# Kernel optimization log

Hardware: AMD Instinct MI355X
Metric: run time of the kernel (lower is better)

## Reference

```python
import jax, jax.numpy as jnp
import numpy as np

B, S, H = 256, 4096, 64

def setup_inputs() -> dict:
    key = jax.random.key(0)
    ks = jax.random.split(key, 6)
    x = jax.random.normal(ks[0], (B, S), dtype=jnp.float32)
    # e = nn.Linear(1, H)
    W_e = jax.random.normal(ks[1], (H, 1), dtype=jnp.float32)
    b_e = jax.random.normal(ks[2], (H,), dtype=jnp.float32) * 0.01
    # PhaseAccumulator learnable per-unit frequency
    omega = 1.0 + 0.1 * jax.random.normal(ks[3], (H,), dtype=jnp.float32)
    # r = nn.Linear(3*H, 1)
    W_r = jax.random.normal(ks[4], (1, 3 * H), dtype=jnp.float32) * (1.0 / np.sqrt(3 * H))
    b_r = jnp.zeros((1,), dtype=jnp.float32)
    return {"x": x, "W_e": W_e, "b_e": b_e, "omega": omega, "W_r": W_r, "b_r": b_r}

def reference(x, W_e, b_e, omega, W_r, b_r):
    # per-step 1->H linear, vectorized over all timesteps: p[b,s,h]
    p = x[:, :, None] * W_e[:, 0] + b_e                 # [B,S,H]
    # xp = stack([cos p, sin p]); accumulator delta = atan2(sin p, cos p) = wrap(p)
    delta = jnp.arctan2(jnp.sin(p), jnp.cos(p))         # [B,S,H], wrapped to (-pi, pi]
    # ph_t = ph_{t-1} + omega * delta_t, ph_0 = 0  ->  cumulative sum over time
    Hseq = jnp.cumsum(omega * delta, axis=1)            # [B,S,H] all phase states
    ph = Hseq[:, -1]                                    # [B,H] final phase
    feat = jnp.concatenate([jnp.cos(ph), jnp.sin(ph), ph], axis=1)  # [B,3H]
    out = feat @ W_r.T + b_r                            # [B,1]
    return out, Hseq
```

## Files before the change

kernel.cpp:

```cpp
#include <hip/hip_runtime.h>

#define B_SZ   256
#define S_SZ   4096
#define H_SZ   64
#define NCHUNK 32
#define CHUNK  (S_SZ / NCHUNK)

#define INV2PI   0.15915494309189535f
#define TWOPI_HI 6.2831854820251465f
#define TWOPI_LO (-1.7484556000744887e-7f)

__device__ __forceinline__ const float* uniform_ptr(const float* p) {
    uint64_t u = (uint64_t)(uintptr_t)p;
    uint32_t lo = __builtin_amdgcn_readfirstlane((uint32_t)u);
    uint32_t hi = __builtin_amdgcn_readfirstlane((uint32_t)(u >> 32));
    return (const float*)(uintptr_t)(((uint64_t)hi << 32) | lo);
}

__global__ __launch_bounds__(256, 4) void k_partials(
    const float* __restrict__ x, const float* __restrict__ W_e,
    const float* __restrict__ b_e, float* __restrict__ ws)
{
    int tid   = blockIdx.x * 256 + threadIdx.x;
    int wid   = tid >> 6;
    int lane  = threadIdx.x & 63;
    int b     = wid >> 5;
    int chunk = wid & (NCHUNK - 1);

    float we = W_e[lane];
    float be = b_e[lane];

    const float* xpu = uniform_ptr(x + b * S_SZ + chunk * CHUNK);
    float accN = 0.f;
    float accX = 0.f;
    #pragma unroll 16
    for (int j = 0; j < CHUNK; ++j) {
        float xs = xpu[j];
        float p  = fmaf(xs, we, be);
        accN += rintf(p * INV2PI);
        accX += xs;
    }
    float sP = fmaf(we, accX, (float)CHUNK * be);
    float d  = fmaf(accN, -TWOPI_HI, sP);
    d        = fmaf(accN, -TWOPI_LO, d);
    ws[wid * 64 + lane] = d;
}

__global__ __launch_bounds__(256, 4) void k_scan(
    const float* __restrict__ x, const float* __restrict__ W_e,
    const float* __restrict__ b_e, const float* __restrict__ omega,
    const float* __restrict__ W_r, const float* __restrict__ b_r,
    const float* __restrict__ ws, float* __restrict__ out,
    float* __restrict__ hseq)
{
    int tid   = blockIdx.x * 256 + threadIdx.x;
    int wid   = tid >> 6;
    int lane  = threadIdx.x & 63;
    int b     = wid >> 5;
    int chunk = wid & (NCHUNK - 1);

    float we = W_e[lane];
    float be = b_e[lane];
    float om = omega[lane];

    float base = 0.f;
    for (int c = 0; c < chunk; ++c)
        base += ws[(b * NCHUNK + c) * 64 + lane];
    float obase = om * base;

    const float* xpu = uniform_ptr(x + b * S_SZ + chunk * CHUNK);
    float* hp = hseq + (size_t)(b * S_SZ + chunk * CHUNK) * H_SZ + lane;

    float acc  = 0.f;
    float Hval = obase;
    #pragma unroll 16
    for (int j = 0; j < CHUNK; ++j) {
        float xs = xpu[j];
        float p  = fmaf(xs, we, be);
        float n  = rintf(p * INV2PI);
        float d0 = fmaf(n, -TWOPI_HI, p);
        d0       = fmaf(n, -TWOPI_LO, d0);
        acc += d0;
        Hval = fmaf(om, acc, obase);
        __builtin_nontemporal_store(Hval, hp + (size_t)j * H_SZ);
    }

    if (chunk == NCHUNK - 1) {
        float ph = Hval;
        float v = cosf(ph) * W_r[lane]
                + sinf(ph) * W_r[H_SZ + lane]
                + ph       * W_r[2 * H_SZ + lane];
        #pragma unroll
        for (int off = 32; off > 0; off >>= 1)
            v += __shfl_down(v, off, 64);
        if (lane == 0) out[b] = v + b_r[0];
    }
}

extern "C" void kernel_launch(void* const* d_in, const int* in_sizes, int n_in,
                              void* d_out, int out_size, void* d_ws, size_t ws_size,
                              hipStream_t stream) {
    const float* x     = (const float*)d_in[0];
    const float* W_e   = (const float*)d_in[1];
    const float* b_e   = (const float*)d_in[2];
    const float* omega = (const float*)d_in[3];
    const float* W_r   = (const float*)d_in[4];
    const float* b_r   = (const float*)d_in[5];

    float* out  = (float*)d_out;
    float* hseq = out + B_SZ;
    float* ws   = (float*)d_ws;

    dim3 blk(256);
    dim3 grid(B_SZ * NCHUNK / 4);

    k_partials<<<grid, blk, 0, stream>>>(x, W_e, b_e, ws);
    k_scan<<<grid, blk, 0, stream>>>(x, W_e, b_e, omega, W_r, b_r, ws, out, hseq);
}
```

Baseline: 296.3 us.

## Fuse partial-sum and scan kernels into one block per batch row using LDS

Replaces the two-kernel chunked scan with a single kernel that processes one whole batch row per 256-thread block. The row of x is staged in LDS, per-chunk wrapped-phase partials are reduced into LDS, and then each wave scans its chunks sequentially. Outputs are transposed through a small LDS buffer so each lane writes float4s. This removes the global workspace round trip, the second launch and the repeated global reads of x. In exchange the grid shrinks to 256 blocks with serial work per wave, which lowers occupancy and the number of stores in flight for a store-bound kernel. The nontemporal store hint is also dropped.

```diff
diff --git a/kernel.cpp b/kernel.cpp
--- a/kernel.cpp
+++ b/kernel.cpp
@@ -5,87 +5,112 @@
 #define H_SZ   64
 #define NCHUNK 32
 #define CHUNK  (S_SZ / NCHUNK)
+#define NWAVE  4
+#define CPW    (NCHUNK / NWAVE)
 
 #define INV2PI   0.15915494309189535f
 #define TWOPI_HI 6.2831854820251465f
 #define TWOPI_LO (-1.7484556000744887e-7f)
 
-__device__ __forceinline__ const float* uniform_ptr(const float* p) {
-    uint64_t u = (uint64_t)(uintptr_t)p;
-    uint32_t lo = __builtin_amdgcn_readfirstlane((uint32_t)u);
-    uint32_t hi = __builtin_amdgcn_readfirstlane((uint32_t)(u >> 32));
-    return (const float*)(uintptr_t)(((uint64_t)hi << 32) | lo);
-}
-
-__global__ __launch_bounds__(256, 4) void k_partials(
-    const float* __restrict__ x, const float* __restrict__ W_e,
-    const float* __restrict__ b_e, float* __restrict__ ws)
-{
-    int tid   = blockIdx.x * 256 + threadIdx.x;
-    int wid   = tid >> 6;
-    int lane  = threadIdx.x & 63;
-    int b     = wid >> 5;
-    int chunk = wid & (NCHUNK - 1);
-
-    float we = W_e[lane];
-    float be = b_e[lane];
-
-    const float* xpu = uniform_ptr(x + b * S_SZ + chunk * CHUNK);
-    float accN = 0.f;
-    float accX = 0.f;
-    #pragma unroll 16
-    for (int j = 0; j < CHUNK; ++j) {
-        float xs = xpu[j];
-        float p  = fmaf(xs, we, be);
-        accN += rintf(p * INV2PI);
-        accX += xs;
-    }
-    float sP = fmaf(we, accX, (float)CHUNK * be);
-    float d  = fmaf(accN, -TWOPI_HI, sP);
-    d        = fmaf(accN, -TWOPI_LO, d);
-    ws[wid * 64 + lane] = d;
-}
-
-__global__ __launch_bounds__(256, 4) void k_scan(
+__global__ __launch_bounds__(256, 2) void k_fused(
     const float* __restrict__ x, const float* __restrict__ W_e,
     const float* __restrict__ b_e, const float* __restrict__ omega,
     const float* __restrict__ W_r, const float* __restrict__ b_r,
-    const float* __restrict__ ws, float* __restrict__ out,
-    float* __restrict__ hseq)
+    float* __restrict__ out, float* __restrict__ hseq)
 {
-    int tid   = blockIdx.x * 256 + threadIdx.x;
-    int wid   = tid >> 6;
-    int lane  = threadIdx.x & 63;
-    int b     = wid >> 5;
-    int chunk = wid & (NCHUNK - 1);
+    __shared__ float lds_x[S_SZ];
+    __shared__ float lds_part[NCHUNK * H_SZ];
+    __shared__ float lds_t[NWAVE * 4 * H_SZ];
 
-    float we = W_e[lane];
-    float be = b_e[lane];
-    float om = omega[lane];
+    const int b    = blockIdx.x;
+    const int tid  = threadIdx.x;
+    const int w    = tid >> 6;
+    const int lane = tid & 63;
+
+    {
+        const float4* xg = (const float4*)(x + (size_t)b * S_SZ);
+        float4* xl = (float4*)lds_x;
+        #pragma unroll
+        for (int k = 0; k < 4; ++k)
+            xl[tid + k * 256] = xg[tid + k * 256];
+    }
+
+    const float we = W_e[lane];
+    const float be = b_e[lane];
+    const float om = omega[lane];
+
+    __syncthreads();
+
+    for (int cc = 0; cc < CPW; ++cc) {
+        const int c = w * CPW + cc;
+        const float4* xl = (const float4*)(lds_x + c * CHUNK);
+        float accN = 0.f;
+        float accX = 0.f;
+        #pragma unroll 4
+        for (int q = 0; q < CHUNK / 4; ++q) {
+            float4 xv = xl[q];
+            { float p = fmaf(xv.x, we, be); accN += rintf(p * INV2PI); accX += xv.x; }
+            { float p = fmaf(xv.y, we, be); accN += rintf(p * INV2PI); accX += xv.y; }
+            { float p = fmaf(xv.z, we, be); accN += rintf(p * INV2PI); accX += xv.z; }
+            { float p = fmaf(xv.w, we, be); accN += rintf(p * INV2PI); accX += xv.w; }
+        }
+        float sP = fmaf(we, accX, (float)CHUNK * be);
+        float d  = fmaf(accN, -TWOPI_HI, sP);
+        d        = fmaf(accN, -TWOPI_LO, d);
+        lds_part[c * H_SZ + lane] = d;
+    }
+
+    __syncthreads();
 
     float base = 0.f;
-    for (int c = 0; c < chunk; ++c)
-        base += ws[(b * NCHUNK + c) * 64 + lane];
-    float obase = om * base;
+    for (int c = 0; c < w * CPW; ++c)
+        base += lds_part[c * H_SZ + lane];
 
-    const float* xpu = uniform_ptr(x + b * S_SZ + chunk * CHUNK);
-    float* hp = hseq + (size_t)(b * S_SZ + chunk * CHUNK) * H_SZ + lane;
+    float* tbuf = lds_t + w * (4 * H_SZ);
+    float Hval = 0.f;
 
-    float acc  = 0.f;
-    float Hval = obase;
-    #pragma unroll 16
-    for (int j = 0; j < CHUNK; ++j) {
-        float xs = xpu[j];
-        float p  = fmaf(xs, we, be);
-        float n  = rintf(p * INV2PI);
-        float d0 = fmaf(n, -TWOPI_HI, p);
-        d0       = fmaf(n, -TWOPI_LO, d0);
-        acc += d0;
-        Hval = fmaf(om, acc, obase);
-        __builtin_nontemporal_store(Hval, hp + (size_t)j * H_SZ);
+    for (int cc = 0; cc < CPW; ++cc) {
+        const int c = w * CPW + cc;
+        const float4* xl = (const float4*)(lds_x + c * CHUNK);
+        float4* gq = (float4*)(hseq + ((size_t)b * S_SZ + c * CHUNK) * H_SZ);
+        const float obase = om * base;
+        float acc = 0.f;
+
+        #pragma unroll 2
+        for (int q = 0; q < CHUNK / 4; ++q) {
+            float4 xv = xl[q];
+            {
+                float p = fmaf(xv.x, we, be); float n = rintf(p * INV2PI);
+                float d0 = fmaf(n, -TWOPI_HI, p); d0 = fmaf(n, -TWOPI_LO, d0);
+                acc += d0; Hval = fmaf(om, acc, obase);
+                tbuf[0 * H_SZ + lane] = Hval;
+            }
+            {
+                float p = fmaf(xv.y, we, be); float n = rintf(p * INV2PI);
+                float d0 = fmaf(n, -TWOPI_HI, p); d0 = fmaf(n, -TWOPI_LO, d0);
+                acc += d0; Hval = fmaf(om, acc, obase);
+                tbuf[1 * H_SZ + lane] = Hval;
+            }
+            {
+                float p = fmaf(xv.z, we, be); float n = rintf(p * INV2PI);
+                float d0 = fmaf(n, -TWOPI_HI, p); d0 = fmaf(n, -TWOPI_LO, d0);
+                acc += d0; Hval = fmaf(om, acc, obase);
+                tbuf[2 * H_SZ + lane] = Hval;
+            }
+            {
+                float p = fmaf(xv.w, we, be); float n = rintf(p * INV2PI);
+                float d0 = fmaf(n, -TWOPI_HI, p); d0 = fmaf(n, -TWOPI_LO, d0);
+                acc += d0; Hval = fmaf(om, acc, obase);
+                tbuf[3 * H_SZ + lane] = Hval;
+            }
+            float4 v = ((const float4*)tbuf)[lane];
+            gq[q * 64 + lane] = v;
+        }
+
+        base += lds_part[c * H_SZ + lane];
     }
 
-    if (chunk == NCHUNK - 1) {
+    if (w == NWAVE - 1) {
         float ph = Hval;
         float v = cosf(ph) * W_r[lane]
                 + sinf(ph) * W_r[H_SZ + lane]
@@ -109,11 +134,7 @@
 
     float* out  = (float*)d_out;
     float* hseq = out + B_SZ;
-    float* ws   = (float*)d_ws;
 
-    dim3 blk(256);
-    dim3 grid(B_SZ * NCHUNK / 4);
-
-    k_partials<<<grid, blk, 0, stream>>>(x, W_e, b_e, ws);
-    k_scan<<<grid, blk, 0, stream>>>(x, W_e, b_e, omega, W_r, b_r, ws, out, hseq);
+    k_fused<<<dim3(B_SZ), dim3(256), 0, stream>>>(
+        x, W_e, b_e, omega, W_r, b_r, out, hseq);
 }
```

New measurement: 279.7 us. 5.6% less time.
